# Optimization experiments

Hardware: AMD Instinct MI355X
Metric: run time of the kernel (lower is better)

## Reference

```python
import jax, jax.numpy as jnp
import numpy as np

DIM = 256
HEADS = 8
DIM_HEAD = 32
INNER = HEADS * DIM_HEAD  # 256
WH, WW = 8, 8
L, H, W = 2, 256, 256
SCALE = DIM_HEAD ** -0.5


def _relative_indices():
    # matches get_relative_distances + offset (window_size - 1)
    idx = np.array([[x, y] for x in range(WH) for y in range(WW)])  # [64, 2]
    dist = idx[None, :, :] - idx[:, None, :]                         # [64, 64, 2]
    return jnp.asarray(dist + np.array([WH - 1, WW - 1]), dtype=jnp.int32)


def setup_inputs() -> dict:
    key = jax.random.key(0)
    ks = jax.random.split(key, 5)
    x = jax.random.normal(ks[0], (L, H, W, DIM), dtype=jnp.float32)
    w_qkv = jax.random.normal(ks[1], (DIM, INNER * 3), dtype=jnp.float32) * (DIM ** -0.5)
    pos_emb = jax.random.normal(ks[2], (2 * WH - 1, 2 * WW - 1), dtype=jnp.float32)
    w_out = jax.random.normal(ks[3], (INNER, DIM), dtype=jnp.float32) * (INNER ** -0.5)
    b_out = jnp.zeros((DIM,), dtype=jnp.float32)
    rel_idx = _relative_indices()  # [64, 64, 2] int32
    return {"x": x, "w_qkv": w_qkv, "pos_emb": pos_emb, "w_out": w_out,
            "b_out": b_out, "rel_idx": rel_idx}


def _to_windows(t):
    # [L, H, W, INNER] -> [L, m, n_windows, window_tokens, dim_head]
    l = t.shape[0]
    nh, nw = H // WH, W // WW
    t = t.reshape(l, nh, WH, nw, WW, HEADS, DIM_HEAD)
    t = t.transpose(0, 5, 1, 3, 2, 4, 6)  # l, m, nh, nw, wh, ww, c
    return t.reshape(l, HEADS, nh * nw, WH * WW, DIM_HEAD)


def _from_windows(t):
    # inverse of _to_windows, merging heads back into channels
    l = t.shape[0]
    nh, nw = H // WH, W // WW
    t = t.reshape(l, HEADS, nh, nw, WH, WW, DIM_HEAD)
    t = t.transpose(0, 2, 4, 3, 5, 1, 6)  # l, nh, wh, nw, ww, m, c
    return t.reshape(l, H, W, INNER)


def reference(x, w_qkv, pos_emb, w_out, b_out, rel_idx):
    qkv = x @ w_qkv                              # [L, H, W, 3*INNER]
    q, k, v = jnp.split(qkv, 3, axis=-1)
    q, k, v = _to_windows(q), _to_windows(k), _to_windows(v)
    dots = jnp.einsum('lmhic,lmhjc->lmhij', q, k) * SCALE
    bias = pos_emb[rel_idx[:, :, 0], rel_idx[:, :, 1]]  # [64, 64]
    attn = jax.nn.softmax(dots + bias, axis=-1)
    out = jnp.einsum('lmhij,lmhjc->lmhic', attn, v)
    out = _from_windows(out)                      # [L, H, W, INNER]
    return out @ w_out + b_out
```

## Files before the change

### kernel.cpp

```cpp
#include <hip/hip_runtime.h>


typedef __bf16 bf16_t;
typedef __bf16 bf16x8 __attribute__((ext_vector_type(8)));
typedef __bf16 bf16x4 __attribute__((ext_vector_type(4)));
typedef float  f32x4  __attribute__((ext_vector_type(4)));

#define MFMA_BF16(a, b, c) __builtin_amdgcn_mfma_f32_16x16x32_bf16((a), (b), (c), 0, 0, 0)
#define SM_SCALE 0.17677669529663687f

#define WPK_OFF   0u
#define WOUTT_OFF 393216u
#define BIASP_OFF 524288u

__global__ __launch_bounds__(256) void prep_kernel(
    const float* __restrict__ w_qkv, const float* __restrict__ w_out,
    const float* __restrict__ pos_emb, const int* __restrict__ rel_idx,
    bf16_t* __restrict__ wpk, bf16_t* __restrict__ woutT,
    float* __restrict__ biasP)
{
    int idx = blockIdx.x * 256 + threadIdx.x;
    if (idx < 196608) {
        int j = idx & 7, lane = (idx >> 3) & 63, t = idx >> 9;
        int ks = t & 7, ni = (t >> 3) & 1, hs = t >> 4;
        int s = hs % 3, h = hs / 3;
        int c = lane & 15, g = lane >> 4;
        int n = s * 256 + h * 32 + ni * 16 + c;
        int k = ks * 32 + g * 8 + j;
        wpk[idx] = (bf16_t)w_qkv[k * 768 + n];
    } else if (idx < 262144) {
        int t = idx - 196608;
        int n = t >> 8, k = t & 255;
        woutT[t] = (bf16_t)w_out[k * 256 + n];
    } else if (idx < 266240) {
        int t = idx - 262144;
        int lane = t >> 6, e = t & 63;
        int ni = e >> 4, mi = (e >> 2) & 3, rg = e & 3;
        int i = 16 * ni + (lane & 15);
        int j = 16 * mi + 4 * (lane >> 4) + rg;
        int i0 = rel_idx[(i * 64 + j) * 2 + 0];
        int i1 = rel_idx[(i * 64 + j) * 2 + 1];
        biasP[t] = pos_emb[i0 * 15 + i1];
    }
}

__global__ __launch_bounds__(512, 2) void fused_kernel(
    const float* __restrict__ x, const bf16_t* __restrict__ wpk,
    const float* __restrict__ biasP, const bf16_t* __restrict__ woutT,
    const float* __restrict__ b_out, float* __restrict__ out)
{
    __shared__ __align__(16) bf16_t XA_s[64 * 256];
    __shared__ __align__(16) bf16_t SB_s[8][2560];

    const int tid = threadIdx.x;
    const int lane = tid & 63, wv = tid >> 6;
    const int g = lane >> 4, c = lane & 15;
    const int b = blockIdx.x;
    const int h = wv;
    const int rbase = (b >> 10) * 65536 + ((b >> 5) & 31) * 2048 + (b & 31) * 8;

    bf16_t* SB = SB_s[wv];
    const float* bp = biasP + lane * 64;
    f32x4 z4 = {0.f, 0.f, 0.f, 0.f};

    const bf16_t* wb0 = wpk + (size_t)((h * 3 + 0) * 2) * 8 * 512;
    bf16x8 bfr[2][8];
#pragma unroll
    for (int ni = 0; ni < 2; ++ni)
#pragma unroll
        for (int ks = 0; ks < 8; ++ks)
            bfr[ni][ks] = *(const bf16x8*)(wb0 + (ni * 8 + ks) * 512 + lane * 8);

#pragma unroll
    for (int jj = 0; jj < 4; ++jj) {
        int q = jj * 512 + tid;
        int tok = q >> 5, ci = q & 31;
        int r = rbase + (tok >> 3) * 256 + (tok & 7);
        const f32x4* xp = (const f32x4*)(x + (size_t)r * 256 + ci * 8);
        f32x4 a = xp[0], bq = xp[1];
        bf16x8 t;
        t[0] = (bf16_t)a[0];  t[1] = (bf16_t)a[1];
        t[2] = (bf16_t)a[2];  t[3] = (bf16_t)a[3];
        t[4] = (bf16_t)bq[0]; t[5] = (bf16_t)bq[1];
        t[6] = (bf16_t)bq[2]; t[7] = (bf16_t)bq[3];
        *(bf16x8*)(XA_s + tok * 256 + ((ci ^ (tok & 31)) << 3)) = t;
    }
    __syncthreads();

    bf16x8 qf[4], kf[4], vbA[2][2];

#pragma unroll
    for (int s = 0; s < 3; ++s) {
        if (s > 0) {
            const bf16_t* wb = wpk + (size_t)((h * 3 + s) * 2) * 8 * 512;
#pragma unroll
            for (int ni = 0; ni < 2; ++ni)
#pragma unroll
                for (int ks = 0; ks < 8; ++ks)
                    bfr[ni][ks] = *(const bf16x8*)(wb + (ni * 8 + ks) * 512 + lane * 8);
        }
        f32x4 acc[4][2];
#pragma unroll
        for (int i = 0; i < 4; ++i) { acc[i][0] = z4; acc[i][1] = z4; }

#pragma unroll
        for (int ks = 0; ks < 8; ++ks) {
            bf16x8 af[4];
#pragma unroll
            for (int mi = 0; mi < 4; ++mi) {
                int tok = 16 * mi + c;
                af[mi] = *(const bf16x8*)(XA_s + tok * 256 + (((4 * ks + g) ^ (tok & 31)) << 3));
            }
#pragma unroll
            for (int mi = 0; mi < 4; ++mi)
#pragma unroll
                for (int ni = 0; ni < 2; ++ni)
                    acc[mi][ni] = MFMA_BF16(af[mi], bfr[ni][ks], acc[mi][ni]);
        }

        if (s < 2) {
#pragma unroll
            for (int mi = 0; mi < 4; ++mi)
#pragma unroll
                for (int ni = 0; ni < 2; ++ni)
#pragma unroll
                    for (int rg = 0; rg < 4; ++rg)
                        SB[(16 * mi + 4 * g + rg) * 40 + 16 * ni + c] =
                            (bf16_t)acc[mi][ni][rg];
            if (s == 0) {
#pragma unroll
                for (int ni2 = 0; ni2 < 4; ++ni2)
                    qf[ni2] = *(const bf16x8*)(SB + (16 * ni2 + c) * 40 + 8 * g);
            } else {
#pragma unroll
                for (int mi2 = 0; mi2 < 4; ++mi2)
                    kf[mi2] = *(const bf16x8*)(SB + (16 * mi2 + c) * 40 + 8 * g);
            }
        } else {
#pragma unroll
            for (int mi = 0; mi < 4; ++mi)
#pragma unroll
                for (int ni = 0; ni < 2; ++ni)
#pragma unroll
                    for (int rg = 0; rg < 4; ++rg)
                        SB[(16 * ni + c) * 72 + (16 * mi + 4 * g + rg)] =
                            (bf16_t)acc[mi][ni][rg];
#pragma unroll
            for (int ks2 = 0; ks2 < 2; ++ks2)
#pragma unroll
                for (int mi2 = 0; mi2 < 2; ++mi2)
                    vbA[ks2][mi2] = *(const bf16x8*)(SB + (16 * mi2 + c) * 72 + 8 * (4 * ks2 + g));
        }
    }
    __syncthreads();

    bf16_t* Pw = SB;
#pragma unroll
    for (int ni = 0; ni < 4; ++ni) {
        f32x4 s[4];
        __builtin_amdgcn_s_setprio(1);
#pragma unroll
        for (int mi = 0; mi < 4; ++mi)
            s[mi] = MFMA_BF16(kf[mi], qf[ni], z4);
        __builtin_amdgcn_s_setprio(0);

        float mx = -1e30f;
#pragma unroll
        for (int mi = 0; mi < 4; ++mi) {
            f32x4 bb = *(const f32x4*)(bp + ni * 16 + mi * 4);
#pragma unroll
            for (int rg = 0; rg < 4; ++rg) {
                float t = fmaf(s[mi][rg], SM_SCALE, bb[rg]);
                s[mi][rg] = t;
                mx = fmaxf(mx, t);
            }
        }
        mx = fmaxf(mx, __shfl_xor(mx, 16));
        mx = fmaxf(mx, __shfl_xor(mx, 32));
        float sm = 0.f;
#pragma unroll
        for (int mi = 0; mi < 4; ++mi)
#pragma unroll
            for (int rg = 0; rg < 4; ++rg) {
                float p = __expf(s[mi][rg] - mx);
                s[mi][rg] = p;
                sm += p;
            }
        sm += __shfl_xor(sm, 16);
        sm += __shfl_xor(sm, 32);
        float inv = 1.0f / sm;

        bf16_t* Pl = Pw + (ni & 1) * 1024;
#pragma unroll
        for (int mi = 0; mi < 4; ++mi) {
            bf16x4 pk;
#pragma unroll
            for (int rg = 0; rg < 4; ++rg) pk[rg] = (bf16_t)s[mi][rg];
            *(bf16x4*)(Pl + c * 64 + (((2 * mi + (g >> 1)) ^ (c & 7)) << 3) + 4 * (g & 1)) = pk;
        }

        f32x4 o0 = z4, o1 = z4;
        __builtin_amdgcn_s_setprio(1);
#pragma unroll
        for (int ks = 0; ks < 2; ++ks) {
            bf16x8 pa = *(const bf16x8*)(Pl + c * 64 + (((4 * ks + g) ^ (c & 7)) << 3));
            o0 = MFMA_BF16(vbA[ks][0], pa, o0);
            o1 = MFMA_BF16(vbA[ks][1], pa, o1);
        }
        __builtin_amdgcn_s_setprio(0);
        int tok = 16 * ni + c;
#pragma unroll
        for (int mi = 0; mi < 2; ++mi) {
            f32x4 ov = (mi == 0) ? o0 : o1;
            bf16x4 pk;
#pragma unroll
            for (int rg = 0; rg < 4; ++rg) pk[rg] = (bf16_t)(ov[rg] * inv);
            int ci = h * 4 + mi * 2 + (g >> 1);
            *(bf16x4*)((char*)XA_s + tok * 512 + ((ci ^ (tok & 31)) << 4) + (g & 1) * 8) = pk;
        }
    }
    __syncthreads();

    f32x4 acc2[4][2];
#pragma unroll
    for (int i = 0; i < 4; ++i) { acc2[i][0] = z4; acc2[i][1] = z4; }

    for (int ks = 0; ks < 8; ++ks) {
        bf16x8 af2[4], bf2[2];
#pragma unroll
        for (int mi = 0; mi < 4; ++mi) {
            int rr = 16 * mi + c;
            af2[mi] = *(const bf16x8*)((char*)XA_s + rr * 512 + (((4 * ks + g) ^ (rr & 31)) << 4));
        }
#pragma unroll
        for (int nj = 0; nj < 2; ++nj)
            bf2[nj] = *(const bf16x8*)(woutT + (size_t)(32 * wv + 16 * nj + c) * 256 + 32 * ks + 8 * g);
#pragma unroll
        for (int mi = 0; mi < 4; ++mi)
#pragma unroll
            for (int nj = 0; nj < 2; ++nj)
                acc2[mi][nj] = MFMA_BF16(af2[mi], bf2[nj], acc2[mi][nj]);
    }

#pragma unroll
    for (int nj = 0; nj < 2; ++nj) {
        int gcol = 32 * wv + 16 * nj + c;
        float bo = b_out[gcol];
#pragma unroll
        for (int mi = 0; mi < 4; ++mi)
#pragma unroll
            for (int rg = 0; rg < 4; ++rg) {
                int tok = 16 * mi + 4 * g + rg;
                size_t r = (size_t)(rbase + (tok >> 3) * 256 + (tok & 7));
                out[r * 256 + gcol] = acc2[mi][nj][rg] + bo;
            }
    }
}

extern "C" void kernel_launch(void* const* d_in, const int* in_sizes, int n_in,
                              void* d_out, int out_size, void* d_ws, size_t ws_size,
                              hipStream_t stream) {
    const float* x       = (const float*)d_in[0];
    const float* w_qkv   = (const float*)d_in[1];
    const float* pos_emb = (const float*)d_in[2];
    const float* w_out   = (const float*)d_in[3];
    const float* b_out   = (const float*)d_in[4];
    const int*   rel_idx = (const int*)d_in[5];

    char* ws = (char*)d_ws;
    bf16_t* wpk   = (bf16_t*)(ws + WPK_OFF);
    bf16_t* woutT = (bf16_t*)(ws + WOUTT_OFF);
    float*  biasP = (float*)(ws + BIASP_OFF);
    float*  out   = (float*)d_out;

    prep_kernel<<<1040, 256, 0, stream>>>(w_qkv, w_out, pos_emb, rel_idx,
                                          wpk, woutT, biasP);
    fused_kernel<<<2048, 512, 0, stream>>>(x, wpk, biasP, woutT, b_out, out);
}
```

Baseline: 154.1 us.

## Halve per-wave LDS staging and raise launch-bounds occupancy target for fused window attention

```diff
diff --git a/kernel.cpp b/kernel.cpp
--- a/kernel.cpp
+++ b/kernel.cpp
@@ -44,13 +44,13 @@
     }
 }
 
-__global__ __launch_bounds__(512, 2) void fused_kernel(
+__global__ __launch_bounds__(512, 6) void fused_kernel(
     const float* __restrict__ x, const bf16_t* __restrict__ wpk,
     const float* __restrict__ biasP, const bf16_t* __restrict__ woutT,
     const float* __restrict__ b_out, float* __restrict__ out)
 {
     __shared__ __align__(16) bf16_t XA_s[64 * 256];
-    __shared__ __align__(16) bf16_t SB_s[8][2560];
+    __shared__ __align__(16) bf16_t SB_s[8][1280];
 
     const int tid = threadIdx.x;
     const int lane = tid & 63, wv = tid >> 6;
@@ -99,57 +99,76 @@
                 for (int ks = 0; ks < 8; ++ks)
                     bfr[ni][ks] = *(const bf16x8*)(wb + (ni * 8 + ks) * 512 + lane * 8);
         }
-        f32x4 acc[4][2];
-#pragma unroll
-        for (int i = 0; i < 4; ++i) { acc[i][0] = z4; acc[i][1] = z4; }
-
-#pragma unroll
-        for (int ks = 0; ks < 8; ++ks) {
-            bf16x8 af[4];
-#pragma unroll
-            for (int mi = 0; mi < 4; ++mi) {
-                int tok = 16 * mi + c;
-                af[mi] = *(const bf16x8*)(XA_s + tok * 256 + (((4 * ks + g) ^ (tok & 31)) << 3));
-            }
-#pragma unroll
-            for (int mi = 0; mi < 4; ++mi)
+
+        if (s < 2) {
+            f32x4 acc[2][4];
+#pragma unroll
+            for (int i = 0; i < 2; ++i)
+#pragma unroll
+                for (int j = 0; j < 4; ++j) acc[i][j] = z4;
+#pragma unroll
+            for (int ks = 0; ks < 8; ++ks) {
+                bf16x8 af[4];
+#pragma unroll
+                for (int mi = 0; mi < 4; ++mi) {
+                    int tok = 16 * mi + c;
+                    af[mi] = *(const bf16x8*)(XA_s + tok * 256 + (((4 * ks + g) ^ (tok & 31)) << 3));
+                }
 #pragma unroll
                 for (int ni = 0; ni < 2; ++ni)
-                    acc[mi][ni] = MFMA_BF16(af[mi], bfr[ni][ks], acc[mi][ni]);
-        }
-
-        if (s < 2) {
-#pragma unroll
-            for (int mi = 0; mi < 4; ++mi)
-#pragma unroll
-                for (int ni = 0; ni < 2; ++ni)
+#pragma unroll
+                    for (int mi = 0; mi < 4; ++mi)
+                        acc[ni][mi] = MFMA_BF16(bfr[ni][ks], af[mi], acc[ni][mi]);
+            }
+            bf16x8* dst = (s == 0) ? qf : kf;
+#pragma unroll
+            for (int half = 0; half < 2; ++half) {
+#pragma unroll
+                for (int mi2 = 0; mi2 < 2; ++mi2)
+#pragma unroll
+                    for (int ni = 0; ni < 2; ++ni) {
+                        bf16x4 pk;
+#pragma unroll
+                        for (int rg = 0; rg < 4; ++rg)
+                            pk[rg] = (bf16_t)acc[ni][2 * half + mi2][rg];
+                        *(bf16x4*)(SB + (16 * mi2 + c) * 40 + 16 * ni + 4 * g) = pk;
+                    }
+#pragma unroll
+                for (int j = 0; j < 2; ++j)
+                    dst[2 * half + j] = *(const bf16x8*)(SB + (16 * j + c) * 40 + 8 * g);
+            }
+        } else {
+            f32x4 acc[4][2];
+#pragma unroll
+            for (int i = 0; i < 4; ++i) { acc[i][0] = z4; acc[i][1] = z4; }
+#pragma unroll
+            for (int ks = 0; ks < 8; ++ks) {
+                bf16x8 af[4];
+#pragma unroll
+                for (int mi = 0; mi < 4; ++mi) {
+                    int tok = 16 * mi + c;
+                    af[mi] = *(const bf16x8*)(XA_s + tok * 256 + (((4 * ks + g) ^ (tok & 31)) << 3));
+                }
+#pragma unroll
+                for (int mi = 0; mi < 4; ++mi)
+#pragma unroll
+                    for (int ni = 0; ni < 2; ++ni)
+                        acc[mi][ni] = MFMA_BF16(af[mi], bfr[ni][ks], acc[mi][ni]);
+            }
+#pragma unroll
+            for (int half = 0; half < 2; ++half) {
+#pragma unroll
+                for (int mi = 0; mi < 4; ++mi) {
+                    bf16x4 pk;
 #pragma unroll
                     for (int rg = 0; rg < 4; ++rg)
-                        SB[(16 * mi + 4 * g + rg) * 40 + 16 * ni + c] =
-                            (bf16_t)acc[mi][ni][rg];
-            if (s == 0) {
-#pragma unroll
-                for (int ni2 = 0; ni2 < 4; ++ni2)
-                    qf[ni2] = *(const bf16x8*)(SB + (16 * ni2 + c) * 40 + 8 * g);
-            } else {
-#pragma unroll
-                for (int mi2 = 0; mi2 < 4; ++mi2)
-                    kf[mi2] = *(const bf16x8*)(SB + (16 * mi2 + c) * 40 + 8 * g);
-            }
-        } else {
-#pragma unroll
-            for (int mi = 0; mi < 4; ++mi)
-#pragma unroll
-                for (int ni = 0; ni < 2; ++ni)
-#pragma unroll
-                    for (int rg = 0; rg < 4; ++rg)
-                        SB[(16 * ni + c) * 72 + (16 * mi + 4 * g + rg)] =
-                            (bf16_t)acc[mi][ni][rg];
-#pragma unroll
-            for (int ks2 = 0; ks2 < 2; ++ks2)
-#pragma unroll
-                for (int mi2 = 0; mi2 < 2; ++mi2)
-                    vbA[ks2][mi2] = *(const bf16x8*)(SB + (16 * mi2 + c) * 72 + 8 * (4 * ks2 + g));
+                        pk[rg] = (bf16_t)acc[mi][half][rg];
+                    *(bf16x4*)(SB + c * 72 + 16 * mi + 4 * g) = pk;
+                }
+#pragma unroll
+                for (int ks2 = 0; ks2 < 2; ++ks2)
+                    vbA[ks2][half] = *(const bf16x8*)(SB + c * 72 + 32 * ks2 + 8 * g);
+            }
         }
     }
     __syncthreads();
@@ -190,7 +209,7 @@
         sm += __shfl_xor(sm, 32);
         float inv = 1.0f / sm;
 
-        bf16_t* Pl = Pw + (ni & 1) * 1024;
+        bf16_t* Pl = Pw;
 #pragma unroll
         for (int mi = 0; mi < 4; ++mi) {
             bf16x4 pk;
```

Measured after the change: 347.9 us. +125.7%, slower.
